# Kernel tuning notes

Measured on AMD Instinct MI355X. Metric: run time of the kernel, lower is better.

The kernel has to match this reference:

```python
import jax, jax.numpy as jnp
import numpy as np

N = 100000
E = 1600000
F_IN = 128
DIM = 32
C = 2
BN_EPS = 1e-5


def setup_inputs() -> dict:
    key = jax.random.key(0)
    ks = jax.random.split(key, 24)
    s = 0.1
    inp = {
        'x': jax.random.normal(ks[0], (N, F_IN), dtype=jnp.float32),
        'edge_index': jax.random.randint(ks[1], (2, E), 0, N, dtype=jnp.int64),
        'edge_attr': jax.random.normal(ks[2], (E, 1), dtype=jnp.float32),
        'batch': jnp.zeros((N,), dtype=jnp.int64),
        # GIN layer 1 MLP: Linear(F_IN, DIM) -> ReLU -> Linear(DIM, DIM)
        'w1a': jax.random.normal(ks[3], (F_IN, DIM), dtype=jnp.float32) * s,
        'b1a': jnp.zeros((DIM,), dtype=jnp.float32),
        'w1b': jax.random.normal(ks[4], (DIM, DIM), dtype=jnp.float32) * s,
        'b1b': jnp.zeros((DIM,), dtype=jnp.float32),
        'g1': jnp.ones((DIM,), dtype=jnp.float32),
        'be1': jnp.zeros((DIM,), dtype=jnp.float32),
        # GIN layer 2
        'w2a': jax.random.normal(ks[5], (DIM, DIM), dtype=jnp.float32) * s,
        'b2a': jnp.zeros((DIM,), dtype=jnp.float32),
        'w2b': jax.random.normal(ks[6], (DIM, DIM), dtype=jnp.float32) * s,
        'b2b': jnp.zeros((DIM,), dtype=jnp.float32),
        'g2': jnp.ones((DIM,), dtype=jnp.float32),
        'be2': jnp.zeros((DIM,), dtype=jnp.float32),
        # GIN layer 3
        'w3a': jax.random.normal(ks[7], (DIM, DIM), dtype=jnp.float32) * s,
        'b3a': jnp.zeros((DIM,), dtype=jnp.float32),
        'w3b': jax.random.normal(ks[8], (DIM, DIM), dtype=jnp.float32) * s,
        'b3b': jnp.zeros((DIM,), dtype=jnp.float32),
        'g3': jnp.ones((DIM,), dtype=jnp.float32),
        'be3': jnp.zeros((DIM,), dtype=jnp.float32),
        # head
        'fw1': jax.random.normal(ks[9], (DIM, DIM), dtype=jnp.float32) * s,
        'fb1': jnp.zeros((DIM,), dtype=jnp.float32),
        'fw2': jax.random.normal(ks[10], (DIM, C), dtype=jnp.float32) * s,
        'fb2': jnp.zeros((C,), dtype=jnp.float32),
    }
    return inp


def _gin(x, src, dst, wa, ba, wb, bb):
    # GINConv with eps=0: h_i = MLP((1+eps)*x_i + sum_{j->i} x_j)
    agg = jax.ops.segment_sum(x[src], dst, num_segments=N)
    h = x + agg
    h = jax.nn.relu(h @ wa + ba) @ wb + bb
    return h


def _bn(h, g, b):
    # BatchNorm1d with batch statistics (training-mode normalization)
    mu = h.mean(axis=0)
    var = h.var(axis=0)  # biased, matches torch normalization
    return (h - mu) * jax.lax.rsqrt(var + BN_EPS) * g + b


def reference(x, edge_index, edge_attr, batch,
              w1a, b1a, w1b, b1b, g1, be1,
              w2a, b2a, w2b, b2b, g2, be2,
              w3a, b3a, w3b, b3b, g3, be3,
              fw1, fb1, fw2, fb2):
    src, dst = edge_index[0], edge_index[1]
    h = _bn(jax.nn.relu(_gin(x, src, dst, w1a, b1a, w1b, b1b)), g1, be1)
    h = _bn(jax.nn.relu(_gin(h, src, dst, w2a, b2a, w2b, b2b)), g2, be2)
    h = _bn(jax.nn.relu(_gin(h, src, dst, w3a, b3a, w3b, b3b)), g3, be3)
    h = jax.nn.relu(h @ fw1 + fb1)
    # dropout treated as identity (eval mode / deterministic reference)
    return h @ fw2 + fb2
```

## Files before the change

kernel.cpp:

```cpp
#include <hip/hip_runtime.h>

#define NNODES 100000
#define NEDGES 1600000
#define FIN 128
#define DIM 32
#define BN_EPS 1e-5f
#define NB_TPN ((NNODES + 255) / 256)
#define NBUK ((NNODES + 255) >> 8)
#define CH 8192

__global__ void __launch_bounds__(256) k_proj1(const float* __restrict__ x,
                                               const float* __restrict__ w,
                                               float* __restrict__ z) {
    const int i = blockIdx.x * 256 + threadIdx.x;
    if (i >= NNODES) return;
    const float4* xp = reinterpret_cast<const float4*>(x + (size_t)i * FIN);
    float acc[DIM];
#pragma unroll
    for (int c = 0; c < DIM; ++c) acc[c] = 0.f;

    for (int k0 = 0; k0 < FIN; k0 += 32) {
        float a[32];
        float4 r[8];
#pragma unroll
        for (int q = 0; q < 8; ++q) r[q] = xp[k0 / 4 + q];
#pragma unroll
        for (int q = 0; q < 8; ++q) {
            a[q * 4 + 0] = r[q].x; a[q * 4 + 1] = r[q].y;
            a[q * 4 + 2] = r[q].z; a[q * 4 + 3] = r[q].w;
        }
#pragma unroll
        for (int kk = 0; kk < 32; ++kk) {
            const float tk = a[kk];
#pragma unroll
            for (int c = 0; c < DIM; ++c)
                acc[c] += tk * w[(k0 + kk) * DIM + c];
        }
    }
    float4* zp = reinterpret_cast<float4*>(z + (size_t)i * DIM);
#pragma unroll
    for (int q = 0; q < 8; ++q)
        zp[q] = make_float4(acc[q * 4], acc[q * 4 + 1], acc[q * 4 + 2], acc[q * 4 + 3]);
}

__global__ void k_bhist(const int* __restrict__ ei, int* __restrict__ bucketCnt) {
    __shared__ int cnt[NBUK];
    for (int i = threadIdx.x; i < NBUK; i += 256) cnt[i] = 0;
    __syncthreads();
    const int tid    = blockIdx.x * blockDim.x + threadIdx.x;
    const int stride = gridDim.x * blockDim.x;
    for (int e = tid; e < NEDGES; e += stride)
        atomicAdd(&cnt[ei[NEDGES + e] >> 8], 1);
    __syncthreads();
    for (int i = threadIdx.x; i < NBUK; i += 256)
        if (cnt[i]) atomicAdd(&bucketCnt[i], cnt[i]);
}

__global__ void k_bscan(const int* __restrict__ bucketCnt,
                        int* __restrict__ bbase, int* __restrict__ gcur) {
    __shared__ int sbuf[512];
    const int t = threadIdx.x;
    const int v = (t < NBUK) ? bucketCnt[t] : 0;
    sbuf[t] = v;
    __syncthreads();
    for (int off = 1; off < 512; off <<= 1) {
        const int u = (t >= off) ? sbuf[t - off] : 0;
        __syncthreads();
        sbuf[t] += u;
        __syncthreads();
    }
    if (t < NBUK) { const int ex = sbuf[t] - v; bbase[t] = ex; gcur[t] = ex; }
    if (t == 0) bbase[NBUK] = NEDGES;
}

__global__ void __launch_bounds__(256) k_bscatter(const int* __restrict__ ei,
                                                  int* __restrict__ gcur,
                                                  int2* __restrict__ bucketed) {
    __shared__ int cnt[NBUK];
    __shared__ int base[NBUK];
    const int start = blockIdx.x * CH;
    const int end   = min(start + CH, NEDGES);
    for (int i = threadIdx.x; i < NBUK; i += 256) cnt[i] = 0;
    __syncthreads();
    for (int e = start + threadIdx.x; e < end; e += 256)
        atomicAdd(&cnt[ei[NEDGES + e] >> 8], 1);
    __syncthreads();
    for (int i = threadIdx.x; i < NBUK; i += 256) {
        const int c = cnt[i];
        base[i] = c ? atomicAdd(&gcur[i], c) : 0;
        cnt[i] = 0;
    }
    __syncthreads();
    for (int e = start + threadIdx.x; e < end; e += 256) {
        const int s = ei[e];
        const int d = ei[NEDGES + e];
        const int b = d >> 8;
        const int p = atomicAdd(&cnt[b], 1);
        bucketed[base[b] + p] = make_int2(s, d);
    }
}

__global__ void __launch_bounds__(256) k_bfill(const int2* __restrict__ bucketed,
                                               const int* __restrict__ bbase,
                                               int* __restrict__ rowstart,
                                               int* __restrict__ deg,
                                               int* __restrict__ sorted_src) {
    __shared__ int dcnt[256], dsc[256], cur[256];
    const int b  = blockIdx.x;
    const int lo = bbase[b];
    const int hi = bbase[b + 1];
    const int n0 = b << 8;
    const int t  = threadIdx.x;
    dcnt[t] = 0;
    __syncthreads();
    for (int p = lo + t; p < hi; p += 256)
        atomicAdd(&dcnt[bucketed[p].y - n0], 1);
    __syncthreads();
    const int myc = dcnt[t];
    dsc[t] = myc;
    __syncthreads();
    for (int off = 1; off < 256; off <<= 1) {
        const int u = (t >= off) ? dsc[t - off] : 0;
        __syncthreads();
        dsc[t] += u;
        __syncthreads();
    }
    const int ex = dsc[t] - myc;
    const int node = n0 + t;
    if (node < NNODES) { rowstart[node] = lo + ex; deg[node] = myc; }
    dcnt[t] = ex;
    cur[t] = 0;
    __syncthreads();
    for (int p = lo + t; p < hi; p += 256) {
        const int2 sd = bucketed[p];
        const int dl = sd.y - n0;
        const int pos = atomicAdd(&cur[dl], 1);
        sorted_src[lo + dcnt[dl] + pos] = sd.x;
    }
}

__global__ void k_gather_t(const float* __restrict__ z,
                           const int* __restrict__ rowstart,
                           const int* __restrict__ deg,
                           const int* __restrict__ sorted_src,
                           const float* __restrict__ ba,
                           float* __restrict__ tbuf) {
    const int lane = threadIdx.x & 31;
    const int g    = lane >> 3;
    const int f4   = lane & 7;
    const float4 ba4 = reinterpret_cast<const float4*>(ba)[f4];
    const int hw  = (blockIdx.x * blockDim.x + threadIdx.x) >> 5;
    const int nhw = (gridDim.x * blockDim.x) >> 5;

    for (int i = hw; i < NNODES; i += nhw) {
        const int base = rowstart[i];
        const int cnt  = deg[i];
        float4 agg0 = make_float4(0.f, 0.f, 0.f, 0.f);
        float4 agg1 = make_float4(0.f, 0.f, 0.f, 0.f);
        for (int k0 = 0; k0 < cnt; k0 += 32) {
            int e = 0;
            if (k0 + lane < cnt) e = sorted_src[base + k0 + lane];
            const int m = min(32, cnt - k0);
            for (int j = 0; j < m; j += 8) {
                const int s0 = __shfl(e, j + g, 32);
                const int s1 = __shfl(e, j + 4 + g, 32);
                if (j + g < m) {
                    const float4 zv = *reinterpret_cast<const float4*>(&z[s0 * DIM + f4 * 4]);
                    agg0.x += zv.x; agg0.y += zv.y; agg0.z += zv.z; agg0.w += zv.w;
                }
                if (j + 4 + g < m) {
                    const float4 zv = *reinterpret_cast<const float4*>(&z[s1 * DIM + f4 * 4]);
                    agg1.x += zv.x; agg1.y += zv.y; agg1.z += zv.z; agg1.w += zv.w;
                }
            }
        }
        agg0.x += agg1.x; agg0.y += agg1.y; agg0.z += agg1.z; agg0.w += agg1.w;
#pragma unroll
        for (int mask = 8; mask <= 16; mask <<= 1) {
            agg0.x += __shfl_xor(agg0.x, mask, 32);
            agg0.y += __shfl_xor(agg0.y, mask, 32);
            agg0.z += __shfl_xor(agg0.z, mask, 32);
            agg0.w += __shfl_xor(agg0.w, mask, 32);
        }
        if (g == 0) {
            const float4 zi = *reinterpret_cast<const float4*>(&z[i * DIM + f4 * 4]);
            float4 t;
            t.x = fmaxf(zi.x + agg0.x + ba4.x, 0.f);
            t.y = fmaxf(zi.y + agg0.y + ba4.y, 0.f);
            t.z = fmaxf(zi.z + agg0.z + ba4.z, 0.f);
            t.w = fmaxf(zi.w + agg0.w + ba4.w, 0.f);
            *reinterpret_cast<float4*>(&tbuf[i * DIM + f4 * 4]) = t;
        }
    }
}

__global__ void __launch_bounds__(256) k_mlp2(float* __restrict__ hbuf,
                                              const float* __restrict__ wb,
                                              const float* __restrict__ bb,
                                              float* __restrict__ stats) {
    __shared__ float ssum[DIM], ssq[DIM];
    if (threadIdx.x < DIM) { ssum[threadIdx.x] = 0.f; ssq[threadIdx.x] = 0.f; }
    __syncthreads();

    const int i = blockIdx.x * 256 + threadIdx.x;
    const bool valid = i < NNODES;

    float a[DIM];
    if (valid) {
        const float4* tp = reinterpret_cast<const float4*>(hbuf + (size_t)i * DIM);
        float4 r[8];
#pragma unroll
        for (int q = 0; q < 8; ++q) r[q] = tp[q];
#pragma unroll
        for (int q = 0; q < 8; ++q) {
            a[q * 4 + 0] = r[q].x; a[q * 4 + 1] = r[q].y;
            a[q * 4 + 2] = r[q].z; a[q * 4 + 3] = r[q].w;
        }
    } else {
#pragma unroll
        for (int k = 0; k < DIM; ++k) a[k] = 0.f;
    }

    float acc[DIM];
#pragma unroll
    for (int c = 0; c < DIM; ++c) acc[c] = bb[c];
#pragma unroll
    for (int k = 0; k < DIM; ++k) {
        const float tk = a[k];
#pragma unroll
        for (int c = 0; c < DIM; ++c)
            acc[c] += tk * wb[k * DIM + c];
    }
#pragma unroll
    for (int c = 0; c < DIM; ++c) acc[c] = valid ? fmaxf(acc[c], 0.f) : 0.f;

    if (valid) {
        float4* hp = reinterpret_cast<float4*>(hbuf + (size_t)i * DIM);
#pragma unroll
        for (int q = 0; q < 8; ++q)
            hp[q] = make_float4(acc[q * 4], acc[q * 4 + 1], acc[q * 4 + 2], acc[q * 4 + 3]);
    }

    const int lane = threadIdx.x & 63;
    float lsum = 0.f, lsq = 0.f;
#pragma unroll
    for (int c = 0; c < DIM; ++c) {
        float v  = acc[c];
        float w2 = acc[c] * acc[c];
#pragma unroll
        for (int off = 1; off < 64; off <<= 1) {
            v  += __shfl_xor(v, off);
            w2 += __shfl_xor(w2, off);
        }
        if (lane == c) { lsum = v; lsq = w2; }
    }
    if (lane < DIM) {
        atomicAdd(&ssum[lane], lsum);
        atomicAdd(&ssq[lane], lsq);
    }
    __syncthreads();
    if (threadIdx.x < DIM) {
        atomicAdd(&stats[threadIdx.x],       ssum[threadIdx.x]);
        atomicAdd(&stats[DIM + threadIdx.x], ssq[threadIdx.x]);
    }
}

__global__ void __launch_bounds__(256) k_projbn(const float* __restrict__ h,
                                                const float* __restrict__ stats,
                                                const float* __restrict__ g,
                                                const float* __restrict__ be,
                                                const float* __restrict__ wa,
                                                float* __restrict__ z) {
    const int i = blockIdx.x * 256 + threadIdx.x;
    if (i >= NNODES) return;
    const float4* hp = reinterpret_cast<const float4*>(h + (size_t)i * DIM);
    float a[DIM];
    float4 r[8];
#pragma unroll
    for (int q = 0; q < 8; ++q) r[q] = hp[q];
#pragma unroll
    for (int q = 0; q < 8; ++q) {
        a[q * 4 + 0] = r[q].x; a[q * 4 + 1] = r[q].y;
        a[q * 4 + 2] = r[q].z; a[q * 4 + 3] = r[q].w;
    }
    float acc[DIM];
#pragma unroll
    for (int c = 0; c < DIM; ++c) acc[c] = 0.f;
#pragma unroll
    for (int k = 0; k < DIM; ++k) {
        const float mu  = stats[k] * (1.f / NNODES);
        const float var = stats[DIM + k] * (1.f / NNODES) - mu * mu;
        const float ss  = g[k] * rsqrtf(var + BN_EPS);
        const float st  = be[k] - mu * ss;
        const float tk  = a[k] * ss + st;
#pragma unroll
        for (int c = 0; c < DIM; ++c)
            acc[c] += tk * wa[k * DIM + c];
    }
    float4* zp = reinterpret_cast<float4*>(z + (size_t)i * DIM);
#pragma unroll
    for (int q = 0; q < 8; ++q)
        zp[q] = make_float4(acc[q * 4], acc[q * 4 + 1], acc[q * 4 + 2], acc[q * 4 + 3]);
}

__global__ void __launch_bounds__(256) k_head(const float* __restrict__ h,
                                              const float* __restrict__ stats,
                                              const float* __restrict__ g,
                                              const float* __restrict__ be,
                                              const float* __restrict__ fw1,
                                              const float* __restrict__ fb1,
                                              const float* __restrict__ fw2,
                                              const float* __restrict__ fb2,
                                              float* __restrict__ out) {
    const int i = blockIdx.x * 256 + threadIdx.x;
    if (i >= NNODES) return;
    const float4* hp = reinterpret_cast<const float4*>(h + (size_t)i * DIM);
    float a[DIM];
    float4 r[8];
#pragma unroll
    for (int q = 0; q < 8; ++q) r[q] = hp[q];
#pragma unroll
    for (int q = 0; q < 8; ++q) {
        a[q * 4 + 0] = r[q].x; a[q * 4 + 1] = r[q].y;
        a[q * 4 + 2] = r[q].z; a[q * 4 + 3] = r[q].w;
    }
    float acc[DIM];
#pragma unroll
    for (int c = 0; c < DIM; ++c) acc[c] = fb1[c];
#pragma unroll
    for (int k = 0; k < DIM; ++k) {
        const float mu  = stats[k] * (1.f / NNODES);
        const float var = stats[DIM + k] * (1.f / NNODES) - mu * mu;
        const float ss  = g[k] * rsqrtf(var + BN_EPS);
        const float st  = be[k] - mu * ss;
        const float tk  = a[k] * ss + st;
#pragma unroll
        for (int c = 0; c < DIM; ++c)
            acc[c] += tk * fw1[k * DIM + c];
    }
    float o0 = fb2[0], o1 = fb2[1];
#pragma unroll
    for (int c = 0; c < DIM; ++c) {
        const float u = fmaxf(acc[c], 0.f);
        o0 += u * fw2[c * 2 + 0];
        o1 += u * fw2[c * 2 + 1];
    }
    *reinterpret_cast<float2*>(&out[i * 2]) = make_float2(o0, o1);
}

extern "C" void kernel_launch(void* const* d_in, const int* in_sizes, int n_in,
                              void* d_out, int out_size, void* d_ws, size_t ws_size,
                              hipStream_t stream) {
    const float* x   = (const float*)d_in[0];
    const int*   ei  = (const int*)d_in[1];
    const float* w1a = (const float*)d_in[4];
    const float* b1a = (const float*)d_in[5];
    const float* w1b = (const float*)d_in[6];
    const float* b1b = (const float*)d_in[7];
    const float* g1  = (const float*)d_in[8];
    const float* be1 = (const float*)d_in[9];
    const float* w2a = (const float*)d_in[10];
    const float* b2a = (const float*)d_in[11];
    const float* w2b = (const float*)d_in[12];
    const float* b2b = (const float*)d_in[13];
    const float* g2  = (const float*)d_in[14];
    const float* be2 = (const float*)d_in[15];
    const float* w3a = (const float*)d_in[16];
    const float* b3a = (const float*)d_in[17];
    const float* w3b = (const float*)d_in[18];
    const float* b3b = (const float*)d_in[19];
    const float* g3  = (const float*)d_in[20];
    const float* be3 = (const float*)d_in[21];
    const float* fw1 = (const float*)d_in[22];
    const float* fb1 = (const float*)d_in[23];
    const float* fw2 = (const float*)d_in[24];
    const float* fb2 = (const float*)d_in[25];
    float* out = (float*)d_out;

    float* ws = (float*)d_ws;
    const size_t nf = (size_t)NNODES * DIM;
    float* z     = ws;
    float* h     = ws + nf;
    int2*  bucketed = (int2*)h;
    float* stats = ws + 2 * nf;
    int* rowstart   = (int*)(ws + 2 * nf + 192);
    int* deg        = rowstart + NNODES;
    int* sorted_src = deg + NNODES;
    int* bucketCnt  = sorted_src + NEDGES;
    int* bbase      = bucketCnt + NBUK;
    int* gcur       = bbase + NBUK + 1;

    const int TB = 256, NB_G = 2048;

    hipMemsetAsync(stats, 0, 3 * 64 * sizeof(float), stream);
    hipMemsetAsync(bucketCnt, 0, NBUK * sizeof(int), stream);

    k_bhist<<<512, TB, 0, stream>>>(ei, bucketCnt);
    k_bscan<<<1, 512, 0, stream>>>(bucketCnt, bbase, gcur);
    k_bscatter<<<(NEDGES + CH - 1) / CH, TB, 0, stream>>>(ei, gcur, bucketed);
    k_bfill<<<NBUK, TB, 0, stream>>>(bucketed, bbase, rowstart, deg, sorted_src);

    k_proj1<<<NB_TPN, TB, 0, stream>>>(x, w1a, z);
    k_gather_t<<<NB_G, TB, 0, stream>>>(z, rowstart, deg, sorted_src, b1a, h);
    k_mlp2<<<NB_TPN, TB, 0, stream>>>(h, w1b, b1b, stats + 0);
    k_projbn<<<NB_TPN, TB, 0, stream>>>(h, stats + 0, g1, be1, w2a, z);
    k_gather_t<<<NB_G, TB, 0, stream>>>(z, rowstart, deg, sorted_src, b2a, h);
    k_mlp2<<<NB_TPN, TB, 0, stream>>>(h, w2b, b2b, stats + 64);
    k_projbn<<<NB_TPN, TB, 0, stream>>>(h, stats + 64, g2, be2, w3a, z);
    k_gather_t<<<NB_G, TB, 0, stream>>>(z, rowstart, deg, sorted_src, b3a, h);
    k_mlp2<<<NB_TPN, TB, 0, stream>>>(h, w3b, b3b, stats + 128);
    k_head<<<NB_TPN, TB, 0, stream>>>(h, stats + 128, g3, be3,
                                      fw1, fb1, fw2, fb2, out);
}
```

Measured before the change: 350.3 us.

## Split-K node matmuls across threads and pack bucketed edges into one int

The per-node dense kernels (proj1, mlp2, projbn, head) now split the reduction dimension across 4 or 2 threads per node. Partial sums are combined through shared memory, which gives more blocks and more memory-level parallelism for the 100k-node matmuls, at the cost of extra shared-memory traffic and a barrier. The bucketed edge array also packs the source index and local destination into a single 32-bit int instead of an int2, halving scatter and fill traffic. The packing assumes source indices fit in 17 bits.

```diff
diff --git a/kernel.cpp b/kernel.cpp
--- a/kernel.cpp
+++ b/kernel.cpp
@@ -5,25 +5,29 @@
 #define FIN 128
 #define DIM 32
 #define BN_EPS 1e-5f
-#define NB_TPN ((NNODES + 255) / 256)
 #define NBUK ((NNODES + 255) >> 8)
 #define CH 8192
 
 __global__ void __launch_bounds__(256) k_proj1(const float* __restrict__ x,
                                                const float* __restrict__ w,
                                                float* __restrict__ z) {
-    const int i = blockIdx.x * 256 + threadIdx.x;
-    if (i >= NNODES) return;
-    const float4* xp = reinterpret_cast<const float4*>(x + (size_t)i * FIN);
+    __shared__ float part[3][64][DIM + 1];
+    const int t  = threadIdx.x;
+    const int nl = t & 63;
+    const int kq = t >> 6;
+    const int i  = blockIdx.x * 64 + nl;
+    const bool valid = i < NNODES;
+
     float acc[DIM];
 #pragma unroll
     for (int c = 0; c < DIM; ++c) acc[c] = 0.f;
 
-    for (int k0 = 0; k0 < FIN; k0 += 32) {
+    if (valid) {
+        const float4* xp = reinterpret_cast<const float4*>(x + (size_t)i * FIN + kq * 32);
+        float4 r[8];
+#pragma unroll
+        for (int q = 0; q < 8; ++q) r[q] = xp[q];
         float a[32];
-        float4 r[8];
-#pragma unroll
-        for (int q = 0; q < 8; ++q) r[q] = xp[k0 / 4 + q];
 #pragma unroll
         for (int q = 0; q < 8; ++q) {
             a[q * 4 + 0] = r[q].x; a[q * 4 + 1] = r[q].y;
@@ -34,13 +38,23 @@
             const float tk = a[kk];
 #pragma unroll
             for (int c = 0; c < DIM; ++c)
-                acc[c] += tk * w[(k0 + kk) * DIM + c];
-        }
-    }
-    float4* zp = reinterpret_cast<float4*>(z + (size_t)i * DIM);
-#pragma unroll
-    for (int q = 0; q < 8; ++q)
-        zp[q] = make_float4(acc[q * 4], acc[q * 4 + 1], acc[q * 4 + 2], acc[q * 4 + 3]);
+                acc[c] += tk * w[(kq * 32 + kk) * DIM + c];
+        }
+    }
+    if (kq > 0) {
+#pragma unroll
+        for (int c = 0; c < DIM; ++c) part[kq - 1][nl][c] = acc[c];
+    }
+    __syncthreads();
+    if (kq == 0 && valid) {
+#pragma unroll
+        for (int c = 0; c < DIM; ++c)
+            acc[c] += part[0][nl][c] + part[1][nl][c] + part[2][nl][c];
+        float4* zp = reinterpret_cast<float4*>(z + (size_t)i * DIM);
+#pragma unroll
+        for (int q = 0; q < 8; ++q)
+            zp[q] = make_float4(acc[q * 4], acc[q * 4 + 1], acc[q * 4 + 2], acc[q * 4 + 3]);
+    }
 }
 
 __global__ void k_bhist(const int* __restrict__ ei, int* __restrict__ bucketCnt) {
@@ -75,7 +89,7 @@
 
 __global__ void __launch_bounds__(256) k_bscatter(const int* __restrict__ ei,
                                                   int* __restrict__ gcur,
-                                                  int2* __restrict__ bucketed) {
+                                                  int* __restrict__ bucketed) {
     __shared__ int cnt[NBUK];
     __shared__ int base[NBUK];
     const int start = blockIdx.x * CH;
@@ -96,11 +110,11 @@
         const int d = ei[NEDGES + e];
         const int b = d >> 8;
         const int p = atomicAdd(&cnt[b], 1);
-        bucketed[base[b] + p] = make_int2(s, d);
-    }
-}
-
-__global__ void __launch_bounds__(256) k_bfill(const int2* __restrict__ bucketed,
+        bucketed[base[b] + p] = s | ((d & 255) << 17);
+    }
+}
+
+__global__ void __launch_bounds__(256) k_bfill(const int* __restrict__ bucketed,
                                                const int* __restrict__ bbase,
                                                int* __restrict__ rowstart,
                                                int* __restrict__ deg,
@@ -109,12 +123,11 @@
     const int b  = blockIdx.x;
     const int lo = bbase[b];
     const int hi = bbase[b + 1];
-    const int n0 = b << 8;
     const int t  = threadIdx.x;
     dcnt[t] = 0;
     __syncthreads();
     for (int p = lo + t; p < hi; p += 256)
-        atomicAdd(&dcnt[bucketed[p].y - n0], 1);
+        atomicAdd(&dcnt[bucketed[p] >> 17], 1);
     __syncthreads();
     const int myc = dcnt[t];
     dsc[t] = myc;
@@ -126,16 +139,16 @@
         __syncthreads();
     }
     const int ex = dsc[t] - myc;
-    const int node = n0 + t;
+    const int node = (b << 8) + t;
     if (node < NNODES) { rowstart[node] = lo + ex; deg[node] = myc; }
     dcnt[t] = ex;
     cur[t] = 0;
     __syncthreads();
     for (int p = lo + t; p < hi; p += 256) {
-        const int2 sd = bucketed[p];
-        const int dl = sd.y - n0;
+        const int v = bucketed[p];
+        const int dl = v >> 17;
         const int pos = atomicAdd(&cur[dl], 1);
-        sorted_src[lo + dcnt[dl] + pos] = sd.x;
+        sorted_src[lo + dcnt[dl] + pos] = v & 0x1FFFF;
     }
 }
 
@@ -198,70 +211,78 @@
                                               const float* __restrict__ wb,
                                               const float* __restrict__ bb,
                                               float* __restrict__ stats) {
+    __shared__ float part[128][DIM + 1];
     __shared__ float ssum[DIM], ssq[DIM];
-    if (threadIdx.x < DIM) { ssum[threadIdx.x] = 0.f; ssq[threadIdx.x] = 0.f; }
-    __syncthreads();
-
-    const int i = blockIdx.x * 256 + threadIdx.x;
+    const int t = threadIdx.x;
+    if (t < DIM) { ssum[t] = 0.f; ssq[t] = 0.f; }
+    const int nl = t & 127;
+    const int kh = t >> 7;
+    const int i  = blockIdx.x * 128 + nl;
     const bool valid = i < NNODES;
 
-    float a[DIM];
+    float a[16];
     if (valid) {
-        const float4* tp = reinterpret_cast<const float4*>(hbuf + (size_t)i * DIM);
-        float4 r[8];
-#pragma unroll
-        for (int q = 0; q < 8; ++q) r[q] = tp[q];
-#pragma unroll
-        for (int q = 0; q < 8; ++q) {
+        const float4* tp = reinterpret_cast<const float4*>(hbuf + (size_t)i * DIM + kh * 16);
+        float4 r[4];
+#pragma unroll
+        for (int q = 0; q < 4; ++q) r[q] = tp[q];
+#pragma unroll
+        for (int q = 0; q < 4; ++q) {
             a[q * 4 + 0] = r[q].x; a[q * 4 + 1] = r[q].y;
             a[q * 4 + 2] = r[q].z; a[q * 4 + 3] = r[q].w;
         }
     } else {
 #pragma unroll
-        for (int k = 0; k < DIM; ++k) a[k] = 0.f;
+        for (int k = 0; k < 16; ++k) a[k] = 0.f;
     }
 
     float acc[DIM];
 #pragma unroll
-    for (int c = 0; c < DIM; ++c) acc[c] = bb[c];
-#pragma unroll
-    for (int k = 0; k < DIM; ++k) {
-        const float tk = a[k];
+    for (int c = 0; c < DIM; ++c) acc[c] = kh ? 0.f : bb[c];
+#pragma unroll
+    for (int kk = 0; kk < 16; ++kk) {
+        const float tk = a[kk];
 #pragma unroll
         for (int c = 0; c < DIM; ++c)
-            acc[c] += tk * wb[k * DIM + c];
-    }
-#pragma unroll
-    for (int c = 0; c < DIM; ++c) acc[c] = valid ? fmaxf(acc[c], 0.f) : 0.f;
-
-    if (valid) {
-        float4* hp = reinterpret_cast<float4*>(hbuf + (size_t)i * DIM);
-#pragma unroll
-        for (int q = 0; q < 8; ++q)
-            hp[q] = make_float4(acc[q * 4], acc[q * 4 + 1], acc[q * 4 + 2], acc[q * 4 + 3]);
-    }
-
-    const int lane = threadIdx.x & 63;
-    float lsum = 0.f, lsq = 0.f;
-#pragma unroll
-    for (int c = 0; c < DIM; ++c) {
-        float v  = acc[c];
-        float w2 = acc[c] * acc[c];
-#pragma unroll
-        for (int off = 1; off < 64; off <<= 1) {
-            v  += __shfl_xor(v, off);
-            w2 += __shfl_xor(w2, off);
-        }
-        if (lane == c) { lsum = v; lsq = w2; }
-    }
-    if (lane < DIM) {
-        atomicAdd(&ssum[lane], lsum);
-        atomicAdd(&ssq[lane], lsq);
-    }
-    __syncthreads();
-    if (threadIdx.x < DIM) {
-        atomicAdd(&stats[threadIdx.x],       ssum[threadIdx.x]);
-        atomicAdd(&stats[DIM + threadIdx.x], ssq[threadIdx.x]);
+            acc[c] += tk * wb[(kh * 16 + kk) * DIM + c];
+    }
+    if (kh) {
+#pragma unroll
+        for (int c = 0; c < DIM; ++c) part[nl][c] = acc[c];
+    }
+    __syncthreads();
+    if (kh == 0) {
+#pragma unroll
+        for (int c = 0; c < DIM; ++c)
+            acc[c] = valid ? fmaxf(acc[c] + part[nl][c], 0.f) : 0.f;
+        if (valid) {
+            float4* hp = reinterpret_cast<float4*>(hbuf + (size_t)i * DIM);
+#pragma unroll
+            for (int q = 0; q < 8; ++q)
+                hp[q] = make_float4(acc[q * 4], acc[q * 4 + 1], acc[q * 4 + 2], acc[q * 4 + 3]);
+        }
+        const int lane = t & 63;
+        float lsum = 0.f, lsq = 0.f;
+#pragma unroll
+        for (int c = 0; c < DIM; ++c) {
+            float v  = acc[c];
+            float w2 = acc[c] * acc[c];
+#pragma unroll
+            for (int off = 1; off < 64; off <<= 1) {
+                v  += __shfl_xor(v, off);
+                w2 += __shfl_xor(w2, off);
+            }
+            if (lane == c) { lsum = v; lsq = w2; }
+        }
+        if (lane < DIM) {
+            atomicAdd(&ssum[lane], lsum);
+            atomicAdd(&ssq[lane], lsq);
+        }
+    }
+    __syncthreads();
+    if (t < DIM) {
+        atomicAdd(&stats[t],       ssum[t]);
+        atomicAdd(&stats[DIM + t], ssq[t]);
     }
 }
 
@@ -271,36 +292,57 @@
                                                 const float* __restrict__ be,
                                                 const float* __restrict__ wa,
                                                 float* __restrict__ z) {
-    const int i = blockIdx.x * 256 + threadIdx.x;
-    if (i >= NNODES) return;
-    const float4* hp = reinterpret_cast<const float4*>(h + (size_t)i * DIM);
-    float a[DIM];
-    float4 r[8];
-#pragma unroll
-    for (int q = 0; q < 8; ++q) r[q] = hp[q];
-#pragma unroll
-    for (int q = 0; q < 8; ++q) {
-        a[q * 4 + 0] = r[q].x; a[q * 4 + 1] = r[q].y;
-        a[q * 4 + 2] = r[q].z; a[q * 4 + 3] = r[q].w;
-    }
+    __shared__ float part[128][DIM + 1];
+    const int t  = threadIdx.x;
+    const int nl = t & 127;
+    const int kh = t >> 7;
+    const int i  = blockIdx.x * 128 + nl;
+    const bool valid = i < NNODES;
+
+    float a[16];
+    if (valid) {
+        const float4* hp = reinterpret_cast<const float4*>(h + (size_t)i * DIM + kh * 16);
+        float4 r[4];
+#pragma unroll
+        for (int q = 0; q < 4; ++q) r[q] = hp[q];
+#pragma unroll
+        for (int q = 0; q < 4; ++q) {
+            a[q * 4 + 0] = r[q].x; a[q * 4 + 1] = r[q].y;
+            a[q * 4 + 2] = r[q].z; a[q * 4 + 3] = r[q].w;
+        }
+    } else {
+#pragma unroll
+        for (int k = 0; k < 16; ++k) a[k] = 0.f;
+    }
+
     float acc[DIM];
 #pragma unroll
     for (int c = 0; c < DIM; ++c) acc[c] = 0.f;
 #pragma unroll
-    for (int k = 0; k < DIM; ++k) {
+    for (int kk = 0; kk < 16; ++kk) {
+        const int k = kh * 16 + kk;
         const float mu  = stats[k] * (1.f / NNODES);
         const float var = stats[DIM + k] * (1.f / NNODES) - mu * mu;
         const float ss  = g[k] * rsqrtf(var + BN_EPS);
         const float st  = be[k] - mu * ss;
-        const float tk  = a[k] * ss + st;
+        const float tk  = a[kk] * ss + st;
 #pragma unroll
         for (int c = 0; c < DIM; ++c)
             acc[c] += tk * wa[k * DIM + c];
     }
-    float4* zp = reinterpret_cast<float4*>(z + (size_t)i * DIM);
-#pragma unroll
-    for (int q = 0; q < 8; ++q)
-        zp[q] = make_float4(acc[q * 4], acc[q * 4 + 1], acc[q * 4 + 2], acc[q * 4 + 3]);
+    if (kh) {
+#pragma unroll
+        for (int c = 0; c < DIM; ++c) part[nl][c] = acc[c];
+    }
+    __syncthreads();
+    if (kh == 0 && valid) {
+#pragma unroll
+        for (int c = 0; c < DIM; ++c) acc[c] += part[nl][c];
+        float4* zp = reinterpret_cast<float4*>(z + (size_t)i * DIM);
+#pragma unroll
+        for (int q = 0; q < 8; ++q)
+            zp[q] = make_float4(acc[q * 4], acc[q * 4 + 1], acc[q * 4 + 2], acc[q * 4 + 3]);
+    }
 }
 
 __global__ void __launch_bounds__(256) k_head(const float* __restrict__ h,
@@ -312,40 +354,59 @@
                                               const float* __restrict__ fw2,
                                               const float* __restrict__ fb2,
                                               float* __restrict__ out) {
-    const int i = blockIdx.x * 256 + threadIdx.x;
-    if (i >= NNODES) return;
-    const float4* hp = reinterpret_cast<const float4*>(h + (size_t)i * DIM);
-    float a[DIM];
-    float4 r[8];
-#pragma unroll
-    for (int q = 0; q < 8; ++q) r[q] = hp[q];
-#pragma unroll
-    for (int q = 0; q < 8; ++q) {
-        a[q * 4 + 0] = r[q].x; a[q * 4 + 1] = r[q].y;
-        a[q * 4 + 2] = r[q].z; a[q * 4 + 3] = r[q].w;
-    }
+    __shared__ float part[128][DIM + 1];
+    const int t  = threadIdx.x;
+    const int nl = t & 127;
+    const int kh = t >> 7;
+    const int i  = blockIdx.x * 128 + nl;
+    const bool valid = i < NNODES;
+
+    float a[16];
+    if (valid) {
+        const float4* hp = reinterpret_cast<const float4*>(h + (size_t)i * DIM + kh * 16);
+        float4 r[4];
+#pragma unroll
+        for (int q = 0; q < 4; ++q) r[q] = hp[q];
+#pragma unroll
+        for (int q = 0; q < 4; ++q) {
+            a[q * 4 + 0] = r[q].x; a[q * 4 + 1] = r[q].y;
+            a[q * 4 + 2] = r[q].z; a[q * 4 + 3] = r[q].w;
+        }
+    } else {
+#pragma unroll
+        for (int k = 0; k < 16; ++k) a[k] = 0.f;
+    }
+
     float acc[DIM];
 #pragma unroll
-    for (int c = 0; c < DIM; ++c) acc[c] = fb1[c];
-#pragma unroll
-    for (int k = 0; k < DIM; ++k) {
+    for (int c = 0; c < DIM; ++c) acc[c] = kh ? 0.f : fb1[c];
+#pragma unroll
+    for (int kk = 0; kk < 16; ++kk) {
+        const int k = kh * 16 + kk;
         const float mu  = stats[k] * (1.f / NNODES);
         const float var = stats[DIM + k] * (1.f / NNODES) - mu * mu;
         const float ss  = g[k] * rsqrtf(var + BN_EPS);
         const float st  = be[k] - mu * ss;
-        const float tk  = a[k] * ss + st;
+        const float tk  = a[kk] * ss + st;
 #pragma unroll
         for (int c = 0; c < DIM; ++c)
             acc[c] += tk * fw1[k * DIM + c];
     }
-    float o0 = fb2[0], o1 = fb2[1];
-#pragma unroll
-    for (int c = 0; c < DIM; ++c) {
-        const float u = fmaxf(acc[c], 0.f);
-        o0 += u * fw2[c * 2 + 0];
-        o1 += u * fw2[c * 2 + 1];
-    }
-    *reinterpret_cast<float2*>(&out[i * 2]) = make_float2(o0, o1);
+    if (kh) {
+#pragma unroll
+        for (int c = 0; c < DIM; ++c) part[nl][c] = acc[c];
+    }
+    __syncthreads();
+    if (kh == 0 && valid) {
+        float o0 = fb2[0], o1 = fb2[1];
+#pragma unroll
+        for (int c = 0; c < DIM; ++c) {
+            const float u = fmaxf(acc[c] + part[nl][c], 0.f);
+            o0 += u * fw2[c * 2 + 0];
+            o1 += u * fw2[c * 2 + 1];
+        }
+        *reinterpret_cast<float2*>(&out[i * 2]) = make_float2(o0, o1);
+    }
 }
 
 extern "C" void kernel_launch(void* const* d_in, const int* in_sizes, int n_in,
@@ -381,7 +442,7 @@
     const size_t nf = (size_t)NNODES * DIM;
     float* z     = ws;
     float* h     = ws + nf;
-    int2*  bucketed = (int2*)h;
+    int*   bucketed = (int*)h;
     float* stats = ws + 2 * nf;
     int* rowstart   = (int*)(ws + 2 * nf + 192);
     int* deg        = rowstart + NNODES;
@@ -391,6 +452,8 @@
     int* gcur       = bbase + NBUK + 1;
 
     const int TB = 256, NB_G = 2048;
+    const int NB_P1 = (NNODES + 63) / 64;
+    const int NB_K2 = (NNODES + 127) / 128;
 
     hipMemsetAsync(stats, 0, 3 * 64 * sizeof(float), stream);
     hipMemsetAsync(bucketCnt, 0, NBUK * sizeof(int), stream);
@@ -400,15 +463,15 @@
     k_bscatter<<<(NEDGES + CH - 1) / CH, TB, 0, stream>>>(ei, gcur, bucketed);
     k_bfill<<<NBUK, TB, 0, stream>>>(bucketed, bbase, rowstart, deg, sorted_src);
 
-    k_proj1<<<NB_TPN, TB, 0, stream>>>(x, w1a, z);
+    k_proj1<<<NB_P1, TB, 0, stream>>>(x, w1a, z);
     k_gather_t<<<NB_G, TB, 0, stream>>>(z, rowstart, deg, sorted_src, b1a, h);
-    k_mlp2<<<NB_TPN, TB, 0, stream>>>(h, w1b, b1b, stats + 0);
-    k_projbn<<<NB_TPN, TB, 0, stream>>>(h, stats + 0, g1, be1, w2a, z);
+    k_mlp2<<<NB_K2, TB, 0, stream>>>(h, w1b, b1b, stats + 0);
+    k_projbn<<<NB_K2, TB, 0, stream>>>(h, stats + 0, g1, be1, w2a, z);
     k_gather_t<<<NB_G, TB, 0, stream>>>(z, rowstart, deg, sorted_src, b2a, h);
-    k_mlp2<<<NB_TPN, TB, 0, stream>>>(h, w2b, b2b, stats + 64);
-    k_projbn<<<NB_TPN, TB, 0, stream>>>(h, stats + 64, g2, be2, w3a, z);
+    k_mlp2<<<NB_K2, TB, 0, stream>>>(h, w2b, b2b, stats + 64);
+    k_projbn<<<NB_K2, TB, 0, stream>>>(h, stats + 64, g2, be2, w3a, z);
     k_gather_t<<<NB_G, TB, 0, stream>>>(z, rowstart, deg, sorted_src, b3a, h);
-    k_mlp2<<<NB_TPN, TB, 0, stream>>>(h, w3b, b3b, stats + 128);
-    k_head<<<NB_TPN, TB, 0, stream>>>(h, stats + 128, g3, be3,
-                                      fw1, fb1, fw2, fb2, out);
-}
+    k_mlp2<<<NB_K2, TB, 0, stream>>>(h, w3b, b3b, stats + 128);
+    k_head<<<NB_K2, TB, 0, stream>>>(h, stats + 128, g3, be3,
+                                     fw1, fb1, fw2, fb2, out);
+}
```

Result: slower. 430.2 us (+22.8%).
